# Kernel optimization log

Hardware: AMD Instinct MI355X
Metric: run time of the kernel (lower is better)

Reference implementation:

```python
import math
import jax, jax.numpy as jnp
import numpy as np

DIM = 4096
N_HEADS = 32
N_KV_HEADS = 8
HEAD_DIM = DIM // N_HEADS        # 128
N_REP = N_HEADS // N_KV_HEADS    # 4
BSZ = 1
SEQ = 2048
ROPE_THETA = 500000.0


def setup_inputs() -> dict:
    key = jax.random.key(0)
    ks = jax.random.split(key, 5)
    scale = 1.0 / math.sqrt(DIM)
    x = jax.random.normal(ks[0], (BSZ, SEQ, DIM), dtype=jnp.float32)
    wq = jax.random.normal(ks[1], (N_HEADS * HEAD_DIM, DIM), dtype=jnp.float32) * scale
    wk = jax.random.normal(ks[2], (N_KV_HEADS * HEAD_DIM, DIM), dtype=jnp.float32) * scale
    wv = jax.random.normal(ks[3], (N_KV_HEADS * HEAD_DIM, DIM), dtype=jnp.float32) * scale
    wo = jax.random.normal(ks[4], (N_HEADS * HEAD_DIM, DIM), dtype=jnp.float32).T * scale
    wo = jnp.asarray(wo)  # [DIM, N_HEADS*HEAD_DIM] like nn.Linear(in=heads*hd, out=dim).weight
    # RoPE tables: freqs_cis[t, j] = exp(i * t * theta^{-2j/head_dim}), j in [0, head_dim/2)
    inv_freq = 1.0 / (ROPE_THETA ** (np.arange(0, HEAD_DIM, 2, dtype=np.float32) / HEAD_DIM))
    t = np.arange(SEQ, dtype=np.float32)
    ang = np.outer(t, inv_freq)  # [SEQ, HEAD_DIM//2]
    freqs_cos = jnp.asarray(np.cos(ang), dtype=jnp.float32)
    freqs_sin = jnp.asarray(np.sin(ang), dtype=jnp.float32)
    # additive causal mask [SEQ, SEQ]
    mask = jnp.where(jnp.tril(jnp.ones((SEQ, SEQ), dtype=bool)), 0.0, -1e9).astype(jnp.float32)
    return {"x": x, "wq": wq, "wk": wk, "wv": wv, "wo": wo,
            "freqs_cos": freqs_cos, "freqs_sin": freqs_sin, "mask": mask}


def _apply_rope(xh, cos, sin):
    # xh: [b, s, h, head_dim]; cos/sin: [s, head_dim//2]
    b, s, h, d = xh.shape
    xr = xh.reshape(b, s, h, d // 2, 2)
    x0, x1 = xr[..., 0], xr[..., 1]
    c = cos[None, :, None, :]
    sn = sin[None, :, None, :]
    o0 = x0 * c - x1 * sn
    o1 = x0 * sn + x1 * c
    return jnp.stack([o0, o1], axis=-1).reshape(b, s, h, d)


def reference(x, wq, wk, wv, wo, freqs_cos, freqs_sin, mask):
    bsz, seqlen, _ = x.shape
    xq = (x @ wq.T).reshape(bsz, seqlen, N_HEADS, HEAD_DIM)
    xk = (x @ wk.T).reshape(bsz, seqlen, N_KV_HEADS, HEAD_DIM)
    xv = (x @ wv.T).reshape(bsz, seqlen, N_KV_HEADS, HEAD_DIM)
    xq = _apply_rope(xq, freqs_cos, freqs_sin)
    xk = _apply_rope(xk, freqs_cos, freqs_sin)
    # repeat_kv (GQA expansion)
    keys = jnp.repeat(xk, N_REP, axis=2)    # [b, s, N_HEADS, hd]
    values = jnp.repeat(xv, N_REP, axis=2)
    scores = jnp.einsum('bqhd,bkhd->bhqk', xq, keys) / math.sqrt(HEAD_DIM)
    scores = scores + mask[None, None, :, :]
    scores = jax.nn.softmax(scores.astype(jnp.float32), axis=-1).astype(xq.dtype)
    out = jnp.einsum('bhqk,bkhd->bqhd', scores, values)
    out = out.reshape(bsz, seqlen, N_HEADS * HEAD_DIM)
    return out @ wo.T
```

## Files before the change

kernel.cpp:

```cpp
#include <hip/hip_runtime.h>
#include <math.h>
#include <stdint.h>
#include <stddef.h>


typedef __attribute__((ext_vector_type(8))) short bf16x8;
typedef __attribute__((ext_vector_type(4))) short bf16x4;
typedef __attribute__((ext_vector_type(4))) float f32x4;
typedef unsigned short u16;

#define NEG_BIG (-1.0e9f)
#define MFMA32(a, b, c) __builtin_amdgcn_mfma_f32_16x16x32_bf16(a, b, c, 0, 0, 0)
#define SFENCE() __builtin_amdgcn_sched_barrier(0)
#define BAR() __builtin_amdgcn_s_barrier()
#define VMW(n_) asm volatile("s_waitcnt vmcnt(" #n_ ")" ::: "memory")

__device__ __forceinline__ float bf2f(u16 b) {
    return __uint_as_float(((unsigned int)b) << 16);
}
__device__ __forceinline__ u16 f2bf(float f) {
    unsigned int u = __float_as_uint(f);
    u += 0x7fff + ((u >> 16) & 1);
    return (u16)(u >> 16);
}
__device__ __forceinline__ void gld_lds16(short* lds, const u16* g) {
    __builtin_amdgcn_global_load_lds(
        (const __attribute__((address_space(1))) void*)g,
        (__attribute__((address_space(3))) void*)lds, 16, 0, 0);
}

__global__ __launch_bounds__(256) void cvt_all(
    const float* __restrict__ x, const float* __restrict__ wq,
    const float* __restrict__ wk, const float* __restrict__ wv,
    const float* __restrict__ wo,
    u16* __restrict__ xb, u16* __restrict__ wqb, u16* __restrict__ wkb,
    u16* __restrict__ wvb, u16* __restrict__ wob) {
    const int b = blockIdx.x;
    const float* s; u16* d; int off;
    if (b < 4096)       { s = x;  d = xb;  off = b; }
    else if (b < 12288) { s = wq; d = wqb; off = b - 4096; }
    else if (b < 14336) { s = wk; d = wkb; off = b - 12288; }
    else if (b < 16384) { s = wv; d = wvb; off = b - 14336; }
    else                { s = wo; d = wob; off = b - 16384; }
    const int i = off * 2048 + threadIdx.x * 8;
    float4 a, c;
    __builtin_memcpy(&a, s + i, 16);
    __builtin_memcpy(&c, s + i + 4, 16);
    bf16x8 o;
    o[0] = (short)f2bf(a.x); o[1] = (short)f2bf(a.y);
    o[2] = (short)f2bf(a.z); o[3] = (short)f2bf(a.w);
    o[4] = (short)f2bf(c.x); o[5] = (short)f2bf(c.y);
    o[6] = (short)f2bf(c.z); o[7] = (short)f2bf(c.w);
    __builtin_memcpy(d + i, &o, 16);
}


#define QSTGA(bf_, ks_, kt_)                                                 \
    { _Pragma("unroll") for (int r_ = 0; r_ < 2; ++r_)                       \
        gld_lds16(Ad + (bf_) * 16384 + (ks_) * 8192 + r_ * 4096,             \
                  Ag + gK * r_ + (size_t)(kt_) * 64 + (ks_) * 32); }
#define QSTGB(bf_, ks_, kt_)                                                 \
    { _Pragma("unroll") for (int r_ = 0; r_ < 2; ++r_)                       \
        gld_lds16(Bd + (bf_) * 16384 + (ks_) * 8192 + r_ * 4096,             \
                  Bg + gK * r_ + (size_t)(kt_) * 64 + (ks_) * 32); }
#define QRDA(bank_, bf_, ks_, mh_)                                           \
    { _Pragma("unroll") for (int i_ = 0; i_ < 4; ++i_)                       \
        __builtin_memcpy(&bank_[i_], S + (bf_) * 16384 + (ks_) * 8192 +      \
                         abase + ((mh_) * 64 + i_ * 16) * 32, 16); }
#define QRDB(bank_, bf_, ks_)                                                \
    { _Pragma("unroll") for (int n_ = 0; n_ < 4; ++n_)                       \
        __builtin_memcpy(&bank_[n_], Bs + (bf_) * 16384 + (ks_) * 8192 +     \
                         bbase + n_ * 512, 16); }
#define QMM(afb_, bfb_, mh_)                                                 \
    {                                                                        \
        __builtin_amdgcn_s_setprio(1);                                       \
        _Pragma("unroll") for (int i_ = 0; i_ < 4; ++i_)                     \
            _Pragma("unroll") for (int n_ = 0; n_ < 4; ++n_)                 \
                acc[(mh_) * 4 + i_][n_] =                                    \
                    MFMA32(afb_[i_], bfb_[n_], acc[(mh_) * 4 + i_][n_]);     \
        __builtin_amdgcn_s_setprio(0);                                       \
    }

template <int OUT>
__device__ __forceinline__ void gemm_q(const u16* __restrict__ A,
                                       const u16* __restrict__ B,
                                       void* __restrict__ C,
                                       int mb, int nb, int N, int K,
                                       short* __restrict__ S) {
    short* const Bs = S + 32768;
    const int t = threadIdx.x;
    const int lane = t & 63, l15 = lane & 15, quad = lane >> 4;
    const int wid = t >> 6, wr = wid >> 2, wc = wid & 3;

    const int srow = t >> 2;
    const int cs = (t & 3) ^ ((t >> 3) & 3);
    const u16* const Ag = A + (size_t)(mb * 256 + srow) * K + cs * 8;
    const u16* const Bg = B + (size_t)(nb * 256 + srow) * K + cs * 8;
    short* const Ad = S + t * 8;
    short* const Bd = Bs + t * 8;
    const size_t gK = (size_t)128 * K;

    const int swz = (quad ^ ((l15 >> 1) & 3)) * 8;
    const int abase = (wr * 128 + l15) * 32 + swz;
    const int bbase = (wc * 64 + l15) * 32 + swz;

    f32x4 acc[8][4] = {};
    bf16x8 af0[4], af1[4], bf0[4], bf1[4];

    QSTGA(0, 0, 0); QSTGB(0, 0, 0);
    QSTGA(0, 1, 0); QSTGB(0, 1, 0);
    QSTGA(1, 0, 1); QSTGB(1, 0, 1);
    VMW(8);
    BAR();
    QRDA(af0, 0, 0, 0); QRDB(bf0, 0, 0);
    SFENCE();

    const int nIt = K >> 7;
    for (int it = 0; it < nIt - 1; ++it) {
        const int k1 = 2 * it + 1, kn0 = 2 * it + 2, kn1 = 2 * it + 3;
        QSTGA(1, 1, k1);  QRDA(af1, 0, 0, 1);                    QMM(af0, bf0, 0); SFENCE(); VMW(6); BAR();
        QSTGB(1, 1, k1);  QRDA(af0, 0, 1, 0); QRDB(bf1, 0, 1);   QMM(af1, bf0, 1); SFENCE();         BAR();
        QSTGA(0, 0, kn0); QRDA(af1, 0, 1, 1);                    QMM(af0, bf1, 0); SFENCE(); VMW(6); BAR();
        QSTGB(0, 0, kn0); QRDA(af0, 1, 0, 0); QRDB(bf0, 1, 0);   QMM(af1, bf1, 1); SFENCE();         BAR();
        QSTGA(0, 1, kn0); QRDA(af1, 1, 0, 1);                    QMM(af0, bf0, 0); SFENCE(); VMW(6); BAR();
        QSTGB(0, 1, kn0); QRDA(af0, 1, 1, 0); QRDB(bf1, 1, 1);   QMM(af1, bf0, 1); SFENCE();         BAR();
        QSTGA(1, 0, kn1); QRDA(af1, 1, 1, 1);                    QMM(af0, bf1, 0); SFENCE(); VMW(6); BAR();
        QSTGB(1, 0, kn1); QRDA(af0, 0, 0, 0); QRDB(bf0, 0, 0);   QMM(af1, bf1, 1); SFENCE();         BAR();
    }
    {
        const int k1 = 2 * nIt - 1;
        QSTGA(1, 1, k1);  QRDA(af1, 0, 0, 1);                    QMM(af0, bf0, 0); SFENCE(); VMW(6); BAR();
        QSTGB(1, 1, k1);  QRDA(af0, 0, 1, 0); QRDB(bf1, 0, 1);   QMM(af1, bf0, 1); SFENCE();         BAR();
        QRDA(af1, 0, 1, 1);                                      QMM(af0, bf1, 0); SFENCE(); VMW(4); BAR();
        QRDA(af0, 1, 0, 0); QRDB(bf0, 1, 0);                     QMM(af1, bf1, 1); SFENCE();         BAR();
        QRDA(af1, 1, 0, 1);                                      QMM(af0, bf0, 0); SFENCE(); VMW(0); BAR();
        QRDA(af0, 1, 1, 0); QRDB(bf1, 1, 1);                     QMM(af1, bf0, 1); SFENCE();         BAR();
        QRDA(af1, 1, 1, 1);                                      QMM(af0, bf1, 0); SFENCE();         BAR();
        QMM(af1, bf1, 1);
    }

#pragma unroll
    for (int i8 = 0; i8 < 8; ++i8) {
        const int rowb = mb * 256 + wr * 128 + (i8 >> 2) * 64 +
                         (i8 & 3) * 16 + quad * 4;
#pragma unroll
        for (int j = 0; j < 4; ++j) {
            const int col = nb * 256 + wc * 64 + j * 16 + l15;
            if (OUT == 2) {
                bf16x4 v;
#pragma unroll
                for (int r = 0; r < 4; ++r) v[r] = (short)f2bf(acc[i8][j][r]);
                __builtin_memcpy((u16*)C + (size_t)col * 2048 + rowb, &v, 8);
            } else {
#pragma unroll
                for (int r = 0; r < 4; ++r)
                    ((u16*)C)[(size_t)(rowb + r) * N + col] =
                        f2bf(acc[i8][j][r]);
            }
        }
    }
}

__global__ __launch_bounds__(512, 2) void qkv_proj8(
    const u16* __restrict__ x,
    const u16* __restrict__ wq, const u16* __restrict__ wk,
    const u16* __restrict__ wv,
    u16* __restrict__ Q, u16* __restrict__ Kc, u16* __restrict__ Vt) {
    __shared__ __align__(16) short S[65536];
    const int lid = blockIdx.x;
    const int swzb = (lid & 7) * 24 + (lid >> 3);
    const int mb = swzb & 7, y = swzb >> 3;
    if (y < 16)
        gemm_q<0>(x, wq, Q, mb, y, 4096, 4096, S);
    else if (y < 20)
        gemm_q<0>(x, wk, Kc, mb, y - 16, 1024, 4096, S);
    else
        gemm_q<2>(x, wv, Vt, mb, y - 20, 1024, 4096, S);
}


#define OSTG(bf_, ks_, kt_)                                                  \
    {                                                                        \
        gld_lds16(Ad + (bf_) * 8192 + (ks_) * 4096,                          \
                  Ag + (size_t)(kt_) * 64 + (ks_) * 32);                     \
        _Pragma("unroll") for (int r_ = 0; r_ < 2; ++r_)                     \
            gld_lds16(Bd + (bf_) * 16384 + (ks_) * 8192 + r_ * 4096,         \
                      Bg + gK * r_ + (size_t)(kt_) * 64 + (ks_) * 32);       \
    }
#define ORDA(bank_, bf_, ks_)                                                \
    { _Pragma("unroll") for (int i_ = 0; i_ < 4; ++i_)                       \
        __builtin_memcpy(&bank_[i_], S + (bf_) * 8192 + (ks_) * 4096 +       \
                         abase + i_ * 512, 16); }
#define ORDB(bank_, bf_, ks_)                                                \
    { _Pragma("unroll") for (int n_ = 0; n_ < 4; ++n_)                       \
        __builtin_memcpy(&bank_[n_], Bs + (bf_) * 16384 + (ks_) * 8192 +     \
                         bbase + n_ * 512, 16); }
#define OMM(afb_, bfb_)                                                      \
    {                                                                        \
        __builtin_amdgcn_s_setprio(1);                                       \
        _Pragma("unroll") for (int i_ = 0; i_ < 4; ++i_)                     \
            _Pragma("unroll") for (int n_ = 0; n_ < 4; ++n_)                 \
                acc[i_][n_] = MFMA32(afb_[i_], bfb_[n_], acc[i_][n_]);       \
        __builtin_amdgcn_s_setprio(0);                                       \
    }

__global__ __launch_bounds__(512, 2) void oproj8(
    const u16* __restrict__ A, const u16* __restrict__ wo,
    float* __restrict__ out) {
    __shared__ __align__(16) short S[49152];
    short* const Bs = S + 16384;
    const int lid = blockIdx.x;
    const int logical = (lid & 7) * 32 + (lid >> 3);
    const int mb = logical & 15, nb = logical >> 4;

    const int t = threadIdx.x;
    const int lane = t & 63, l15 = lane & 15, quad = lane >> 4;
    const int wid = t >> 6, wr = wid >> 2, wc = wid & 3;

    const int srow = t >> 2;
    const int cs = (t & 3) ^ ((t >> 3) & 3);
    const u16* const Ag = A + (size_t)(mb * 128 + srow) * 4096 + cs * 8;
    const u16* const Bg = wo + (size_t)(nb * 256 + srow) * 4096 + cs * 8;
    short* const Ad = S + t * 8;
    short* const Bd = Bs + t * 8;
    const size_t gK = (size_t)128 * 4096;

    const int swz = (quad ^ ((l15 >> 1) & 3)) * 8;
    const int abase = (wr * 64 + l15) * 32 + swz;
    const int bbase = (wc * 64 + l15) * 32 + swz;

    f32x4 acc[4][4] = {};
    bf16x8 af0[4], af1[4], bf0[4], bf1[4];

    OSTG(0, 0, 0); OSTG(0, 1, 0); OSTG(1, 0, 1);
    VMW(3);
    BAR();
    ORDA(af0, 0, 0); ORDB(bf0, 0, 0);
    SFENCE();

    const int nIt = 32;
    for (int it = 0; it < nIt - 1; ++it) {
        const int k1 = 2 * it + 1, kn0 = 2 * it + 2, kn1 = 2 * it + 3;
        OSTG(1, 1, k1);  ORDA(af1, 0, 1); ORDB(bf1, 0, 1); OMM(af0, bf0); SFENCE(); VMW(3); BAR();
        OSTG(0, 0, kn0); ORDA(af0, 1, 0); ORDB(bf0, 1, 0); OMM(af1, bf1); SFENCE(); VMW(3); BAR();
        OSTG(0, 1, kn0); ORDA(af1, 1, 1); ORDB(bf1, 1, 1); OMM(af0, bf0); SFENCE(); VMW(3); BAR();
        OSTG(1, 0, kn1); ORDA(af0, 0, 0); ORDB(bf0, 0, 0); OMM(af1, bf1); SFENCE(); VMW(3); BAR();
    }
    {
        const int k1 = 2 * nIt - 1;
        OSTG(1, 1, k1);  ORDA(af1, 0, 1); ORDB(bf1, 0, 1); OMM(af0, bf0); SFENCE(); VMW(3); BAR();
        ORDA(af0, 1, 0); ORDB(bf0, 1, 0);                  OMM(af1, bf1); SFENCE(); VMW(0); BAR();
        ORDA(af1, 1, 1); ORDB(bf1, 1, 1);                  OMM(af0, bf0); SFENCE();         BAR();
        OMM(af1, bf1);
    }

#pragma unroll
    for (int i = 0; i < 4; ++i) {
        const int rowb = mb * 128 + wr * 64 + i * 16 + quad * 4;
#pragma unroll
        for (int j = 0; j < 4; ++j) {
            const int col = nb * 256 + wc * 64 + j * 16 + l15;
#pragma unroll
            for (int r = 0; r < 4; ++r)
                out[(size_t)(rowb + r) * 4096 + col] = acc[i][j][r];
        }
    }
}

__global__ __launch_bounds__(256) void rope_all(
    u16* __restrict__ Q, u16* __restrict__ Kc,
    const float* __restrict__ cosb, const float* __restrict__ sinb) {
    const int idx = blockIdx.x * blockDim.x + threadIdx.x;
    const int i = idx & 63;
    const int hh = (idx >> 6) % 40;
    const int s = (idx >> 6) / 40;
    u16* p;
    if (hh < 32)
        p = Q + (size_t)s * 4096 + hh * 128 + 2 * i;
    else
        p = Kc + (size_t)s * 1024 + (hh - 32) * 128 + 2 * i;
    const float x0 = bf2f(p[0]), x1 = bf2f(p[1]);
    const float c = cosb[s * 64 + i], sn = sinb[s * 64 + i];
    p[0] = f2bf(x0 * c - x1 * sn);
    p[1] = f2bf(x0 * sn + x1 * c);
}

__device__ __forceinline__ int kswz(int row, int cs) {
    int f = (row & 3) | ((row & 8) >> 1);
    return row * 128 + ((cs ^ f) << 3);
}

template <bool MASKED>
__device__ __forceinline__ void fa_step_lds(
    const short* __restrict__ Kl, const short* __restrict__ Vl,
    int kb, int q0, int l15, int quad,
    const int (&koff)[8], const int (&voff)[8],
    const bf16x8 (&qf)[4], f32x4 (&o)[8], float& m, float& l) {
    const float scale = 0.08838834764831845f;

    bf16x8 kf[8];
#pragma unroll
    for (int i = 0; i < 8; ++i) __builtin_memcpy(&kf[i], Kl + koff[i], 16);
    f32x4 s0 = {0, 0, 0, 0}, s1 = {0, 0, 0, 0};
#pragma unroll
    for (int c = 0; c < 4; ++c) {
        s0 = MFMA32(kf[c], qf[c], s0);
        s1 = MFMA32(kf[4 + c], qf[c], s1);
    }

    bf16x8 vf[8];
#pragma unroll
    for (int n = 0; n < 8; ++n) __builtin_memcpy(&vf[n], Vl + voff[n], 16);

    float sv0[4], sv1[4];
    const int q = q0 + l15;
#pragma unroll
    for (int r = 0; r < 4; ++r) {
        sv0[r] = s0[r] * scale;
        sv1[r] = s1[r] * scale;
        if (MASKED) {
            if (kb + 8 * quad + r > q) sv0[r] = NEG_BIG;
            if (kb + 8 * quad + 4 + r > q) sv1[r] = NEG_BIG;
        }
    }

    float mx = fmaxf(fmaxf(fmaxf(sv0[0], sv0[1]), fmaxf(sv0[2], sv0[3])),
                     fmaxf(fmaxf(sv1[0], sv1[1]), fmaxf(sv1[2], sv1[3])));
    mx = fmaxf(mx, __shfl_xor(mx, 16));
    mx = fmaxf(mx, __shfl_xor(mx, 32));

    float alpha = 1.0f;
    if (!__all(mx <= m + 8.0f)) {
        float mnew = fmaxf(m, mx);
        alpha = __expf(m - mnew);
        float aO[4];
#pragma unroll
        for (int r = 0; r < 4; ++r) aO[r] = __shfl(alpha, quad * 20 + r);
#pragma unroll
        for (int n = 0; n < 8; ++n)
#pragma unroll
            for (int r = 0; r < 4; ++r) o[n][r] *= aO[r];
        m = mnew;
    }

    float p0[4], p1[4], sum = 0.f;
#pragma unroll
    for (int r = 0; r < 4; ++r) {
        p0[r] = __expf(sv0[r] - m);
        p1[r] = __expf(sv1[r] - m);
        sum += p0[r] + p1[r];
    }
    sum += __shfl_xor(sum, 16);
    sum += __shfl_xor(sum, 32);
    l = l * alpha + sum;

    bf16x8 pa;
#pragma unroll
    for (int r = 0; r < 4; ++r) {
        pa[r] = (short)f2bf(p0[r]);
        pa[4 + r] = (short)f2bf(p1[r]);
    }

#pragma unroll
    for (int n = 0; n < 8; ++n) o[n] = MFMA32(pa, vf[n], o[n]);
}

__device__ __forceinline__ void fa_task(
    const u16* __restrict__ Q, const u16* __restrict__ Kc,
    const u16* __restrict__ Vt, u16* __restrict__ O,
    short* __restrict__ Kl0, short* __restrict__ Vl0,
    int q0, int nbt, int h, int kvh, int t) {
    const int lane = t & 63;
    const int l15 = lane & 15, quad = lane >> 4;

    bf16x8 qf[4];
    const u16* qp = Q + (size_t)(q0 + l15) * 4096 + h * 128 + quad * 8;
#pragma unroll
    for (int c = 0; c < 4; ++c) __builtin_memcpy(&qf[c], qp + c * 32, 16);

    const u16* ksrc[2]; short* kdst[2];
    const u16* vsrc[2]; short* vdst[2];
#pragma unroll
    for (int r = 0; r < 2; ++r) {
        int row = (t >> 4) + 16 * r;
        int slot = t & 15;
        int f = (row & 3) | ((row & 8) >> 1);
        int cks = slot ^ f;
        ksrc[r] = Kc + (size_t)row * 1024 + kvh * 128 + cks * 8;
        kdst[r] = Kl0 + (t + 256 * r) * 8;
        int rowv = (t >> 2) + 64 * r;
        int csv = (t & 3) ^ ((t >> 3) & 3);
        vsrc[r] = Vt + (size_t)(kvh * 128 + rowv) * 2048 + csv * 8;
        vdst[r] = Vl0 + (t + 256 * r) * 8;
    }

    const int rk0 = 8 * (l15 >> 2) + (l15 & 3);
    int koff[8], voff[8];
#pragma unroll
    for (int c = 0; c < 4; ++c) {
        koff[c] = kswz(rk0, quad + c * 4);
        koff[4 + c] = kswz(rk0 + 4, quad + c * 4);
    }
    const int vswz = (quad ^ ((l15 >> 1) & 3)) * 8;
#pragma unroll
    for (int n = 0; n < 8; ++n) voff[n] = (n * 16 + l15) * 32 + vswz;

    f32x4 o[8] = {};
    float m = NEG_BIG, l = 0.f;
    const int my_nb = (q0 + 47) / 32;

    {
        gld_lds16(kdst[0], ksrc[0]);
        gld_lds16(kdst[1], ksrc[1]);
        gld_lds16(vdst[0], vsrc[0]);
        gld_lds16(vdst[1], vsrc[1]);
    }
    __syncthreads();

    for (int ib = 0; ib < nbt; ++ib) {
        if (ib + 1 < nbt) {
            int kb = (ib + 1) * 32;
            int bo = ((ib + 1) & 1) * 4096;
            gld_lds16(kdst[0] + bo, ksrc[0] + (size_t)kb * 1024);
            gld_lds16(kdst[1] + bo, ksrc[1] + (size_t)kb * 1024);
            gld_lds16(vdst[0] + bo, vsrc[0] + kb);
            gld_lds16(vdst[1] + bo, vsrc[1] + kb);
        }
        if (ib < my_nb) {
            const short* Kl = Kl0 + (ib & 1) * 4096;
            const short* Vl = Vl0 + (ib & 1) * 4096;
            if (ib == my_nb - 1)
                fa_step_lds<true>(Kl, Vl, ib * 32, q0, l15, quad, koff, voff,
                                  qf, o, m, l);
            else
                fa_step_lds<false>(Kl, Vl, ib * 32, q0, l15, quad, koff, voff,
                                   qf, o, m, l);
        }
        __syncthreads();
    }

    float inv[4];
#pragma unroll
    for (int r = 0; r < 4; ++r) inv[r] = 1.f / __shfl(l, quad * 20 + r);
#pragma unroll
    for (int n = 0; n < 8; ++n)
#pragma unroll
        for (int r = 0; r < 4; ++r) {
            int row = q0 + quad * 4 + r;
            O[(size_t)row * 4096 + h * 128 + n * 16 + l15] =
                f2bf(o[n][r] * inv[r]);
        }
}

__global__ __launch_bounds__(256) void flash_attn(
    const u16* __restrict__ Q, const u16* __restrict__ Kc,
    const u16* __restrict__ Vt, u16* __restrict__ O) {
    __shared__ __align__(16) short Kl[2 * 32 * 128];
    __shared__ __align__(16) short Vl[2 * 128 * 32];
    const int pp = blockIdx.x;
    const int h = blockIdx.y;
    const int kvh = h >> 2;
    const int t = threadIdx.x, wave = t >> 6;
    fa_task(Q, Kc, Vt, O, Kl, Vl, pp * 64 + wave * 16, 2 * pp + 2, h, kvh, t);
    const int tb = 31 - pp;
    fa_task(Q, Kc, Vt, O, Kl, Vl, tb * 64 + (3 - wave) * 16, 2 * tb + 2, h,
            kvh, t);
}

extern "C" void kernel_launch(void* const* d_in, const int* in_sizes, int n_in,
                              void* d_out, int out_size, void* d_ws,
                              size_t ws_size, hipStream_t stream) {
    const float* x  = (const float*)d_in[0];
    const float* wq = (const float*)d_in[1];
    const float* wk = (const float*)d_in[2];
    const float* wv = (const float*)d_in[3];
    const float* wo = (const float*)d_in[4];
    const float* fc = (const float*)d_in[5];
    const float* fs = (const float*)d_in[6];
    float* out = (float*)d_out;

    const int NX = 2048 * 4096;
    const int NQW = 4096 * 4096;
    const int NKW = 1024 * 4096;
    const int NKV = 2048 * 1024;

    u16* Q   = (u16*)d_ws;
    u16* Kc  = Q   + NX;
    u16* Vt  = Kc  + NKV;
    u16* Ao  = Vt  + NKV;
    u16* xb  = Ao  + NX;
    u16* wqb = xb  + NX;
    u16* wkb = wqb + NQW;
    u16* wvb = wkb + NKW;
    u16* wob = wvb + NKW;

    cvt_all<<<24576, 256, 0, stream>>>(x, wq, wk, wv, wo,
                                       xb, wqb, wkb, wvb, wob);
    qkv_proj8<<<192, 512, 0, stream>>>(xb, wqb, wkb, wvb, Q, Kc, Vt);
    rope_all<<<20480, 256, 0, stream>>>(Q, Kc, fc, fs);
    flash_attn<<<dim3(16, 32), 256, 0, stream>>>(Q, Kc, Vt, Ao);
    oproj8<<<256, 512, 0, stream>>>(Ao, wob, out);
}
```

Before: 512.6 us.

## Restructure oproj pipeline to single fragment bank and widen flash-attn KV tiles to 64

The output-projection GEMM drops its double-buffered register fragment banks. Each phase now loads A/B fragments, issues the next global-to-LDS stage, then synchronises with barriers and lgkmcnt waits around the MFMA block, which lowers register pressure but adds barriers. Flash attention now stages 64-key K/V blocks per iteration instead of 32, with a wider V swizzle, two 32-key sub-steps per block, and a 2-block occupancy hint. This halves the number of syncthreads per KV sweep but doubles LDS use.

```diff
diff --git a/kernel.cpp b/kernel.cpp
--- a/kernel.cpp
+++ b/kernel.cpp
@@ -179,7 +179,7 @@
 }
 
 
-#define OSTG(bf_, ks_, kt_)                                                  \
+#define O8_STG(bf_, ks_, kt_)                                                \
     {                                                                        \
         gld_lds16(Ad + (bf_) * 8192 + (ks_) * 4096,                          \
                   Ag + (size_t)(kt_) * 64 + (ks_) * 32);                     \
@@ -187,21 +187,27 @@
             gld_lds16(Bd + (bf_) * 16384 + (ks_) * 8192 + r_ * 4096,         \
                       Bg + gK * r_ + (size_t)(kt_) * 64 + (ks_) * 32);       \
     }
-#define ORDA(bank_, bf_, ks_)                                                \
-    { _Pragma("unroll") for (int i_ = 0; i_ < 4; ++i_)                       \
-        __builtin_memcpy(&bank_[i_], S + (bf_) * 8192 + (ks_) * 4096 +       \
-                         abase + i_ * 512, 16); }
-#define ORDB(bank_, bf_, ks_)                                                \
-    { _Pragma("unroll") for (int n_ = 0; n_ < 4; ++n_)                       \
-        __builtin_memcpy(&bank_[n_], Bs + (bf_) * 16384 + (ks_) * 8192 +     \
-                         bbase + n_ * 512, 16); }
-#define OMM(afb_, bfb_)                                                      \
+#define O8_PHASE(bf_, ks_, STAGE_, WAIT_)                                    \
     {                                                                        \
+        _Pragma("unroll") for (int n_ = 0; n_ < 4; ++n_)                     \
+            __builtin_memcpy(&bfr[n_], Bs + (bf_) * 16384 + (ks_) * 8192 +   \
+                                           bbase + n_ * 512, 16);            \
+        _Pragma("unroll") for (int i_ = 0; i_ < 4; ++i_)                     \
+            __builtin_memcpy(&af[i_], S + (bf_) * 8192 + (ks_) * 4096 +      \
+                                          abase + i_ * 512, 16);             \
+        STAGE_;                                                              \
+        SFENCE();                                                            \
+        __builtin_amdgcn_s_barrier();                                        \
+        asm volatile("s_waitcnt lgkmcnt(0)" ::: "memory");                   \
+        SFENCE();                                                            \
         __builtin_amdgcn_s_setprio(1);                                       \
         _Pragma("unroll") for (int i_ = 0; i_ < 4; ++i_)                     \
             _Pragma("unroll") for (int n_ = 0; n_ < 4; ++n_)                 \
-                acc[i_][n_] = MFMA32(afb_[i_], bfb_[n_], acc[i_][n_]);       \
+                acc[i_][n_] = MFMA32(af[i_], bfr[n_], acc[i_][n_]);          \
         __builtin_amdgcn_s_setprio(0);                                       \
+        SFENCE();                                                            \
+        WAIT_;                                                               \
+        __builtin_amdgcn_s_barrier();                                        \
     }
 
 __global__ __launch_bounds__(512, 2) void oproj8(
@@ -230,28 +236,26 @@
     const int bbase = (wc * 64 + l15) * 32 + swz;
 
     f32x4 acc[4][4] = {};
-    bf16x8 af0[4], af1[4], bf0[4], bf1[4];
-
-    OSTG(0, 0, 0); OSTG(0, 1, 0); OSTG(1, 0, 1);
-    VMW(3);
+    bf16x8 af[4], bfr[4];
+
+    O8_STG(0, 0, 0); O8_STG(0, 1, 0); O8_STG(1, 0, 1);
+    VMW(6);
     BAR();
-    ORDA(af0, 0, 0); ORDB(bf0, 0, 0);
-    SFENCE();
 
     const int nIt = 32;
     for (int it = 0; it < nIt - 1; ++it) {
         const int k1 = 2 * it + 1, kn0 = 2 * it + 2, kn1 = 2 * it + 3;
-        OSTG(1, 1, k1);  ORDA(af1, 0, 1); ORDB(bf1, 0, 1); OMM(af0, bf0); SFENCE(); VMW(3); BAR();
-        OSTG(0, 0, kn0); ORDA(af0, 1, 0); ORDB(bf0, 1, 0); OMM(af1, bf1); SFENCE(); VMW(3); BAR();
-        OSTG(0, 1, kn0); ORDA(af1, 1, 1); ORDB(bf1, 1, 1); OMM(af0, bf0); SFENCE(); VMW(3); BAR();
-        OSTG(1, 0, kn1); ORDA(af0, 0, 0); ORDB(bf0, 0, 0); OMM(af1, bf1); SFENCE(); VMW(3); BAR();
+        O8_PHASE(0, 0, O8_STG(1, 1, k1),  VMW(6));
+        O8_PHASE(0, 1, O8_STG(0, 0, kn0), VMW(6));
+        O8_PHASE(1, 0, O8_STG(0, 1, kn0), VMW(6));
+        O8_PHASE(1, 1, O8_STG(1, 0, kn1), VMW(6));
     }
     {
         const int k1 = 2 * nIt - 1;
-        OSTG(1, 1, k1);  ORDA(af1, 0, 1); ORDB(bf1, 0, 1); OMM(af0, bf0); SFENCE(); VMW(3); BAR();
-        ORDA(af0, 1, 0); ORDB(bf0, 1, 0);                  OMM(af1, bf1); SFENCE(); VMW(0); BAR();
-        ORDA(af1, 1, 1); ORDB(bf1, 1, 1);                  OMM(af0, bf0); SFENCE();         BAR();
-        OMM(af1, bf1);
+        O8_PHASE(0, 0, O8_STG(1, 1, k1), VMW(6));
+        O8_PHASE(0, 1, ,                 VMW(3));
+        O8_PHASE(1, 0, ,                 VMW(0));
+        O8_PHASE(1, 1, , );
     }
 
 #pragma unroll
@@ -293,14 +297,15 @@
 template <bool MASKED>
 __device__ __forceinline__ void fa_step_lds(
     const short* __restrict__ Kl, const short* __restrict__ Vl,
-    int kb, int q0, int l15, int quad,
+    int kb, int kadd, int q0, int l15, int quad,
     const int (&koff)[8], const int (&voff)[8],
     const bf16x8 (&qf)[4], f32x4 (&o)[8], float& m, float& l) {
     const float scale = 0.08838834764831845f;
 
     bf16x8 kf[8];
 #pragma unroll
-    for (int i = 0; i < 8; ++i) __builtin_memcpy(&kf[i], Kl + koff[i], 16);
+    for (int i = 0; i < 8; ++i)
+        __builtin_memcpy(&kf[i], Kl + koff[i] + kadd, 16);
     f32x4 s0 = {0, 0, 0, 0}, s1 = {0, 0, 0, 0};
 #pragma unroll
     for (int c = 0; c < 4; ++c) {
@@ -369,7 +374,7 @@
     const u16* __restrict__ Q, const u16* __restrict__ Kc,
     const u16* __restrict__ Vt, u16* __restrict__ O,
     short* __restrict__ Kl0, short* __restrict__ Vl0,
-    int q0, int nbt, int h, int kvh, int t) {
+    int q0, int nbt64, int h, int kvh, int t) {
     const int lane = t & 63;
     const int l15 = lane & 15, quad = lane >> 4;
 
@@ -378,63 +383,72 @@
 #pragma unroll
     for (int c = 0; c < 4; ++c) __builtin_memcpy(&qf[c], qp + c * 32, 16);
 
-    const u16* ksrc[2]; short* kdst[2];
-    const u16* vsrc[2]; short* vdst[2];
-#pragma unroll
-    for (int r = 0; r < 2; ++r) {
+    const u16* ksrc[4]; short* kdst[4];
+    const u16* vsrc[4]; short* vdst[4];
+#pragma unroll
+    for (int r = 0; r < 4; ++r) {
         int row = (t >> 4) + 16 * r;
         int slot = t & 15;
         int f = (row & 3) | ((row & 8) >> 1);
         int cks = slot ^ f;
         ksrc[r] = Kc + (size_t)row * 1024 + kvh * 128 + cks * 8;
         kdst[r] = Kl0 + (t + 256 * r) * 8;
-        int rowv = (t >> 2) + 64 * r;
-        int csv = (t & 3) ^ ((t >> 3) & 3);
+        int rowv = (t >> 3) + 32 * r;
+        int csv = (t & 7) ^ ((t >> 3) & 7);
         vsrc[r] = Vt + (size_t)(kvh * 128 + rowv) * 2048 + csv * 8;
         vdst[r] = Vl0 + (t + 256 * r) * 8;
     }
 
     const int rk0 = 8 * (l15 >> 2) + (l15 & 3);
-    int koff[8], voff[8];
+    int koff[8], voff0[8], voff1[8];
 #pragma unroll
     for (int c = 0; c < 4; ++c) {
         koff[c] = kswz(rk0, quad + c * 4);
         koff[4 + c] = kswz(rk0 + 4, quad + c * 4);
     }
-    const int vswz = (quad ^ ((l15 >> 1) & 3)) * 8;
-#pragma unroll
-    for (int n = 0; n < 8; ++n) voff[n] = (n * 16 + l15) * 32 + vswz;
+#pragma unroll
+    for (int n = 0; n < 8; ++n) {
+        const int row = n * 16 + l15;
+        voff0[n] = row * 64 + ((quad ^ (l15 & 7)) << 3);
+        voff1[n] = row * 64 + (((quad + 4) ^ (l15 & 7)) << 3);
+    }
 
     f32x4 o[8] = {};
     float m = NEG_BIG, l = 0.f;
-    const int my_nb = (q0 + 47) / 32;
-
-    {
-        gld_lds16(kdst[0], ksrc[0]);
-        gld_lds16(kdst[1], ksrc[1]);
-        gld_lds16(vdst[0], vsrc[0]);
-        gld_lds16(vdst[1], vsrc[1]);
+    const int my_nb32 = (q0 + 47) / 32;
+
+#pragma unroll
+    for (int r = 0; r < 4; ++r) {
+        gld_lds16(kdst[r], ksrc[r]);
+        gld_lds16(vdst[r], vsrc[r]);
     }
     __syncthreads();
 
-    for (int ib = 0; ib < nbt; ++ib) {
-        if (ib + 1 < nbt) {
-            int kb = (ib + 1) * 32;
-            int bo = ((ib + 1) & 1) * 4096;
-            gld_lds16(kdst[0] + bo, ksrc[0] + (size_t)kb * 1024);
-            gld_lds16(kdst[1] + bo, ksrc[1] + (size_t)kb * 1024);
-            gld_lds16(vdst[0] + bo, vsrc[0] + kb);
-            gld_lds16(vdst[1] + bo, vsrc[1] + kb);
+    for (int ib = 0; ib < nbt64; ++ib) {
+        if (ib + 1 < nbt64) {
+            const int kb = (ib + 1) * 64;
+            const int bo = ((ib + 1) & 1) * 8192;
+#pragma unroll
+            for (int r = 0; r < 4; ++r) {
+                gld_lds16(kdst[r] + bo, ksrc[r] + (size_t)kb * 1024);
+                gld_lds16(vdst[r] + bo, vsrc[r] + kb);
+            }
         }
-        if (ib < my_nb) {
-            const short* Kl = Kl0 + (ib & 1) * 4096;
-            const short* Vl = Vl0 + (ib & 1) * 4096;
-            if (ib == my_nb - 1)
-                fa_step_lds<true>(Kl, Vl, ib * 32, q0, l15, quad, koff, voff,
-                                  qf, o, m, l);
-            else
-                fa_step_lds<false>(Kl, Vl, ib * 32, q0, l15, quad, koff, voff,
-                                   qf, o, m, l);
+        const short* Kl = Kl0 + (ib & 1) * 8192;
+        const short* Vl = Vl0 + (ib & 1) * 8192;
+#pragma unroll
+        for (int sub = 0; sub < 2; ++sub) {
+            const int ib32 = 2 * ib + sub;
+            if (ib32 < my_nb32) {
+                const int kb = ib * 64 + sub * 32;
+                const int kadd = sub * 4096;
+                if (ib32 == my_nb32 - 1)
+                    fa_step_lds<true>(Kl, Vl, kb, kadd, q0, l15, quad, koff,
+                                      sub ? voff1 : voff0, qf, o, m, l);
+                else
+                    fa_step_lds<false>(Kl, Vl, kb, kadd, q0, l15, quad, koff,
+                                       sub ? voff1 : voff0, qf, o, m, l);
+            }
         }
         __syncthreads();
     }
@@ -452,18 +466,18 @@
         }
 }
 
-__global__ __launch_bounds__(256) void flash_attn(
+__global__ __launch_bounds__(256, 2) void flash_attn(
     const u16* __restrict__ Q, const u16* __restrict__ Kc,
     const u16* __restrict__ Vt, u16* __restrict__ O) {
-    __shared__ __align__(16) short Kl[2 * 32 * 128];
-    __shared__ __align__(16) short Vl[2 * 128 * 32];
+    __shared__ __align__(16) short Kl[2 * 64 * 128];
+    __shared__ __align__(16) short Vl[2 * 128 * 64];
     const int pp = blockIdx.x;
     const int h = blockIdx.y;
     const int kvh = h >> 2;
     const int t = threadIdx.x, wave = t >> 6;
-    fa_task(Q, Kc, Vt, O, Kl, Vl, pp * 64 + wave * 16, 2 * pp + 2, h, kvh, t);
+    fa_task(Q, Kc, Vt, O, Kl, Vl, pp * 64 + wave * 16, pp + 1, h, kvh, t);
     const int tb = 31 - pp;
-    fa_task(Q, Kc, Vt, O, Kl, Vl, tb * 64 + (3 - wave) * 16, 2 * tb + 2, h,
+    fa_task(Q, Kc, Vt, O, Kl, Vl, tb * 64 + (3 - wave) * 16, tb + 1, h,
             kvh, t);
 }
 
```

Measured after the change: 471.7 us. 1.09x faster.
